# Kernel optimization log

Hardware: AMD Instinct MI355X
Metric: run time of the kernel (lower is better)

Reference implementation:

```python
import jax, jax.numpy as jnp
import numpy as np

B, L, H, HEADS, DK = 256, 20, 128, 8, 16
NT, NR = 4, 4
CHILD, PARENT = 30001, 500
N1S, N1D, E1 = 50000, 20000, 300000
N2, E2 = 20000, 200000
T = B * L
N4D, E4 = 5000, 150000
EC2P = 8000
D2 = H // 2  # gamma=0.5 split for diachronic embedding


def _ln(x):
    m = jnp.mean(x, -1, keepdims=True)
    v = jnp.var(x, -1, keepdims=True)
    return (x - m) * jax.lax.rsqrt(v + 1e-5)


def _tmod(h, w, b):
    # temporal modulation with per-node diachronic params (activ='sin')
    return jnp.concatenate([h[..., :D2], h[..., D2:] * jnp.sin(w[..., D2:] + b[..., D2:])], -1)


def _dia(e, w, b, t):
    t = t[..., None].astype(e.dtype)
    return jnp.concatenate([e[..., :D2], e[..., D2:] * jnp.sin(w[..., D2:] * t + b[..., D2:])], -1)


def _typed(x, t, W):
    # type-conditioned linear: W [NT, in, out]; small NT -> compute all, select
    y = jnp.einsum('nh,tho->tno', x, W)
    return y[t, jnp.arange(x.shape[0])]


def _seg_softmax(s, seg, n):
    m = jax.ops.segment_max(s, seg, num_segments=n)
    m = jnp.where(jnp.isfinite(m), m, 0.0)
    ex = jnp.exp(s - m[seg])
    den = jax.ops.segment_sum(ex, seg, num_segments=n)
    return ex / jnp.maximum(den[seg], 1e-9)


def _htgt(src_h, src_t, tw, tb, eh, esrc, edst, etype, dst_h, dst_t, KW, QW, VW, OW, EW, mu):
    # relational multi-head attention on a bipartite block (HTGTLayer, pre_norm)
    nd = dst_h.shape[0]
    hs = _tmod(_ln(src_h), tw, tb)
    k = _typed(hs, src_t, KW).reshape(-1, HEADS, DK)
    v = _typed(hs, src_t, VW).reshape(-1, HEADS, DK)
    q = _typed(_ln(dst_h), dst_t, QW).reshape(nd, HEADS, DK)
    ke = k[esrc] + (eh @ EW).reshape(-1, HEADS, DK)
    score = (q[edst] * ke).sum(-1) * mu[etype] / np.float32(np.sqrt(DK))  # [E, HEADS]
    a = _seg_softmax(score, edst, nd)
    agg = jax.ops.segment_sum(a[..., None] * v[esrc], edst, num_segments=nd).reshape(nd, H)
    return _typed(agg, dst_t, OW) + dst_h


def _lstm(x, Wi, Wh, b):
    h0 = jnp.zeros((x.shape[0], H), x.dtype)
    def step(carry, xt):
        h, c = carry
        g = xt @ Wi + h @ Wh + b
        i, f, gg, o = jnp.split(g, 4, -1)
        c = jax.nn.sigmoid(f) * c + jax.nn.sigmoid(i) * jnp.tanh(gg)
        h = jax.nn.sigmoid(o) * jnp.tanh(c)
        return (h, c), h
    _, hs = jax.lax.scan(step, (h0, h0), jnp.swapaxes(x, 0, 1))
    return jnp.swapaxes(hs, 0, 1)


def _forward(seq, seq_ntype, dur, stime, etime, g1_nid, g1_ntype, g1_esrc, g1_edst, g1_etype, g1_ew,
             g2_src_sel, g2_esrc, g2_edst, g2_etype, g2_ew, tok_sel, g4_esrc, g4_edst, g4_etype, g4_ew,
             pe_p, pe_c, emb, hist_emb, edge_emb, dia_w, dia_b, t2v_w, t2v_b, exp_W, exp_b,
             lstm1_Wi, lstm1_Wh, lstm1_b, lstm2_Wi, lstm2_Wh, lstm2_b,
             convK, convQ, convV, convO, convE, convMu, ipW, iaW, skip):
    # ---- sequence module ----
    e0 = emb[seq]
    st = _dia(e0, dia_w[seq], dia_b[seq], stime)
    et = _dia(e0, dia_w[seq], dia_b[seq], etime)
    t = dur[..., None].astype(jnp.float32)
    tv = jnp.concatenate([t2v_w[:1] * t + t2v_b[:1], jnp.sin(t2v_w[1:] * t + t2v_b[1:])], -1)
    x = jax.nn.relu(jnp.concatenate([st, et, tv], -1) @ exp_W + exp_b)
    h1 = _lstm(x, lstm1_Wi, lstm1_Wh, lstm1_b)
    his = jnp.swapaxes(h1, 0, 1).reshape(T, H)  # packed (time-major) token states
    tok_id = jnp.swapaxes(seq, 0, 1).reshape(T)
    tok_nt = jnp.swapaxes(seq_ntype, 0, 1).reshape(T)
    # ---- conv1 (g2g) on block 1 ----
    sh1 = emb[g1_nid]
    xg = jax.nn.relu(_htgt(sh1, g1_ntype, dia_w[g1_nid], dia_b[g1_nid], edge_emb[g1_ew],
                           g1_esrc, g1_edst, g1_etype, sh1[:N1D], g1_ntype[:N1D],
                           convK[0], convQ[0], convV[0], convO[0], convE[0], convMu[0]))
    # ---- conv2 (g2s): graph nodes -> packed sequence tokens ----
    gnid2 = g1_nid[g2_src_sel]
    dst_h2 = xg[tok_sel] + his
    x2 = jax.nn.relu(_htgt(xg[g2_src_sel], g1_ntype[g2_src_sel], dia_w[gnid2], dia_b[gnid2], edge_emb[g2_ew],
                           g2_esrc, g2_edst, g2_etype, dst_h2, tok_nt,
                           convK[1], convQ[1], convV[1], convO[1], convE[1], convMu[1]))
    seq2 = jnp.swapaxes(x2.reshape(L, B, H), 0, 1)
    h2 = _lstm(seq2, lstm2_Wi, lstm2_Wh, lstm2_b)  # final seq_embed
    # ---- individual pooling (attn) + history push ----
    ent = jnp.swapaxes(h2, 0, 1).reshape(T, H)
    a = _typed(jnp.tanh(_typed(ent, tok_nt, ipW)), tok_nt, iaW)[:, 0]
    w = _seg_softmax(a, tok_id, CHILD)
    node_embed = jax.ops.segment_sum(w[:, None] * ent, tok_id, num_segments=CHILD)
    cnt = jax.ops.segment_sum(jnp.ones((T,), jnp.float32), tok_id, num_segments=CHILD)
    hist2 = jnp.where(cnt[:, None] > 0, node_embed, hist_emb)
    # ---- graph module: conv3, conv4 with skip-gated pull ----
    alpha = jax.nn.sigmoid(skip)[g1_ntype][:, None]
    x0 = emb[g1_nid] * alpha + hist2[g1_nid] * (1.0 - alpha)
    x3 = jax.nn.relu(_htgt(x0, g1_ntype, dia_w[g1_nid], dia_b[g1_nid], edge_emb[g1_ew],
                           g1_esrc, g1_edst, g1_etype, x0[:N1D], g1_ntype[:N1D],
                           convK[2], convQ[2], convV[2], convO[2], convE[2], convMu[2]))
    nid4 = g1_nid[:N1D]
    child_embed = _htgt(x3, g1_ntype[:N1D], dia_w[nid4], dia_b[nid4], edge_emb[g4_ew],
                        g4_esrc, g4_edst, g4_etype, x3[:N4D], g1_ntype[:N4D],
                        convK[3], convQ[3], convV[3], convO[3], convE[3], convMu[3])
    # ---- parent pooling (avg over c2p map) ----
    psum = jax.ops.segment_sum(child_embed[pe_c], pe_p, num_segments=PARENT)
    pcnt = jax.ops.segment_sum(jnp.ones((EC2P,), jnp.float32), pe_p, num_segments=PARENT)
    parent_embed = psum / jnp.maximum(pcnt, 1.0)[:, None]
    return (h2, child_embed, parent_embed)


def setup_inputs() -> dict:
    key = jax.random.key(0)
    ks = iter(jax.random.split(key, 64))
    def ri(shape, hi):
        return jax.random.randint(next(ks), shape, 0, hi, dtype=jnp.int32)
    def rn(shape, s=0.02):
        return jax.random.normal(next(ks), shape, dtype=jnp.float32) * s
    return dict(
        seq=ri((B, L), CHILD), seq_ntype=ri((B, L), NT), dur=ri((B, L), 40),
        stime=ri((B, L), 60), etime=ri((B, L), 60),
        g1_nid=ri((N1S,), CHILD), g1_ntype=ri((N1S,), NT),
        g1_esrc=ri((E1,), N1S), g1_edst=ri((E1,), N1D), g1_etype=ri((E1,), NR), g1_ew=ri((E1,), 50),
        g2_src_sel=ri((N2,), N1D), g2_esrc=ri((E2,), N2), g2_edst=ri((E2,), T),
        g2_etype=ri((E2,), NR), g2_ew=ri((E2,), 50),
        tok_sel=ri((T,), N1D),
        g4_esrc=ri((E4,), N1D), g4_edst=ri((E4,), N4D), g4_etype=ri((E4,), NR), g4_ew=ri((E4,), 50),
        pe_p=ri((EC2P,), PARENT), pe_c=ri((EC2P,), N4D),
        emb=rn((CHILD, H), 0.05), hist_emb=rn((CHILD, H), 0.05), edge_emb=rn((50, 32), 0.05),
        dia_w=rn((CHILD, H), 0.05), dia_b=rn((CHILD, H), 0.05),
        t2v_w=rn((16,), 0.1), t2v_b=rn((16,), 0.1),
        exp_W=rn((2 * H + 16, H)), exp_b=jnp.zeros((H,), jnp.float32),
        lstm1_Wi=rn((H, 4 * H)), lstm1_Wh=rn((H, 4 * H)), lstm1_b=jnp.zeros((4 * H,), jnp.float32),
        lstm2_Wi=rn((H, 4 * H)), lstm2_Wh=rn((H, 4 * H)), lstm2_b=jnp.zeros((4 * H,), jnp.float32),
        convK=rn((4, NT, H, H)), convQ=rn((4, NT, H, H)), convV=rn((4, NT, H, H)), convO=rn((4, NT, H, H)),
        convE=rn((4, 32, H)), convMu=jnp.ones((4, NR, HEADS), jnp.float32),
        ipW=rn((NT, H, H)), iaW=rn((NT, H, 1)), skip=jnp.ones((NT,), jnp.float32),
    )


def reference(seq, seq_ntype, dur, stime, etime, g1_nid, g1_ntype, g1_esrc, g1_edst, g1_etype, g1_ew,
              g2_src_sel, g2_esrc, g2_edst, g2_etype, g2_ew, tok_sel, g4_esrc, g4_edst, g4_etype, g4_ew,
              pe_p, pe_c, emb, hist_emb, edge_emb, dia_w, dia_b, t2v_w, t2v_b, exp_W, exp_b,
              lstm1_Wi, lstm1_Wh, lstm1_b, lstm2_Wi, lstm2_Wh, lstm2_b,
              convK, convQ, convV, convO, convE, convMu, ipW, iaW, skip):
    return _forward(seq, seq_ntype, dur, stime, etime, g1_nid, g1_ntype, g1_esrc, g1_edst, g1_etype, g1_ew,
                    g2_src_sel, g2_esrc, g2_edst, g2_etype, g2_ew, tok_sel, g4_esrc, g4_edst, g4_etype, g4_ew,
                    pe_p, pe_c, emb, hist_emb, edge_emb, dia_w, dia_b, t2v_w, t2v_b, exp_W, exp_b,
                    lstm1_Wi, lstm1_Wh, lstm1_b, lstm2_Wi, lstm2_Wh, lstm2_b,
                    convK, convQ, convV, convO, convE, convMu, ipW, iaW, skip)
```

## Files before the change

### kernel.cpp

```cpp
#include <hip/hip_runtime.h>
#include <math.h>

#define BB 256
#define LL 20
#define HH 128
#define NH 8
#define D2C 64
#define NTY 4
#define NRL 4
#define CHILDN 30001
#define PARENTN 500
#define N1SN 50000
#define N1DN 20000
#define E1N 300000
#define N2N 20000
#define E2N 200000
#define TT (BB*LL)
#define N4DN 5000
#define E4N 150000
#define EC2PN 8000
#define TDSTRIDE 2304

typedef __attribute__((ext_vector_type(8))) short bfrag;
typedef __attribute__((ext_vector_type(4))) float ffrag;

__device__ __forceinline__ unsigned fenc(float f){ unsigned u=__float_as_uint(f); return (u&0x80000000u)? ~u : (u|0x80000000u); }
__device__ __forceinline__ float fdec(unsigned u){ return (u&0x80000000u)? __uint_as_float(u^0x80000000u) : __uint_as_float(~u); }
__device__ __forceinline__ float sigfast(float x){ return 1.f/(1.f+__expf(-x)); }
__device__ __forceinline__ float tanhfast(float x){ float e = __expf(-2.f*x); return (1.f-e)/(1.f+e); }
__device__ __forceinline__ short f2bf(float f){
  unsigned u = __float_as_uint(f);
  unsigned r = u + 0x7FFFu + ((u>>16)&1u);
  return (short)(r>>16);
}

__global__ void k_init(float* hist2, float* cnt, unsigned* amax, float* aden,
                       float* psum, float* pcnt, int* cntall,
                       int* icnt1, int* icnt2, int* icnt3,
                       const float* __restrict__ dia_w, const float* __restrict__ dia_b,
                       float* __restrict__ sdia,
                       const float* convK, const float* convV, const float* convQ,
                       const float* convO, short* Wsw,
                       const float* edge_emb, const float* convE, float* EW2all){
  int i = blockIdx.x*256 + threadIdx.x;
  if(i < CHILDN*HH) hist2[i] = 0.f;
  if(i < CHILDN){ cnt[i] = 0.f; aden[i] = 0.f; amax[i] = 0x007FFFFFu; }
  if(i < PARENTN*HH) psum[i] = 0.f;
  if(i < PARENTN) pcnt[i] = 0.f;
  if(i < 5*NTY) cntall[i] = 0;
  if(i < N1DN) icnt1[i] = 0;
  if(i < TT)   icnt2[i] = 0;
  if(i < N4DN) icnt3[i] = 0;
  if(i < CHILDN*64){
    int c = i >> 6, k = (i & 63) + 64;
    sdia[i] = __sinf(dia_w[(size_t)c*HH+k] + dia_b[(size_t)c*HH+k]);
  }
  if(i < 64*16384){
    int m = i >> 14, im = i & 16383;
    int fam = m >> 4, lt = m & 15;
    const float* src = (fam==0?convK:fam==1?convV:fam==2?convQ:convO) + (size_t)lt*HH*HH;
    int j = im & 7, lane = (im>>3)&63, kc = (im>>9)&3, nt = im>>11;
    int k = kc*32 + (lane>>4)*8 + j;
    int n = nt*16 + (lane&15);
    Wsw[(size_t)m*16384 + im] = f2bf(src[k*HH+n]);
  }
  if(i < 4*50*HH){
    int layer = i/(50*HH), rr = (i/HH)%50, o = i%HH;
    const float* EWp = convE + (size_t)layer*32*HH;
    float acc = 0.f;
    for(int j=0;j<32;j++) acc += edge_emb[rr*32+j]*EWp[j*HH+o];
    EW2all[i] = acc;
  }
}

__global__ __launch_bounds__(512) void k_featx2(const int* __restrict__ seq, const int* __restrict__ dur,
                        const int* __restrict__ stime, const int* __restrict__ etime,
                        const float* __restrict__ emb, const float* __restrict__ dia_w, const float* __restrict__ dia_b,
                        const float* __restrict__ t2v_w, const float* __restrict__ t2v_b,
                        const float* __restrict__ exp_W, const float* __restrict__ exp_b, float* __restrict__ xout){
  __shared__ float feat[32*273];
  int base = blockIdx.x*32;
  int j = threadIdx.x >> 4;
  int p = threadIdx.x & 15;
  int row = base + j;
  int node = seq[row];
  float ts = (float)stime[row], te = (float)etime[row];
  const float* ep = emb + (size_t)node*HH;
  float* fr = feat + j*273;
  int o0 = p*8;
  #pragma unroll
  for(int ii=0; ii<8; ii+=4){
    int o = o0 + ii;
    float4 e = *(const float4*)(ep + o);
    float4 st = e, et = e;
    if(o >= D2C){
      float4 w = *(const float4*)(dia_w + (size_t)node*HH + o);
      float4 b = *(const float4*)(dia_b + (size_t)node*HH + o);
      st.x = e.x*__sinf(w.x*ts+b.x); st.y = e.y*__sinf(w.y*ts+b.y);
      st.z = e.z*__sinf(w.z*ts+b.z); st.w = e.w*__sinf(w.w*ts+b.w);
      et.x = e.x*__sinf(w.x*te+b.x); et.y = e.y*__sinf(w.y*te+b.y);
      et.z = e.z*__sinf(w.z*te+b.z); et.w = e.w*__sinf(w.w*te+b.w);
    }
    fr[o] = st.x; fr[o+1] = st.y; fr[o+2] = st.z; fr[o+3] = st.w;
    fr[128+o] = et.x; fr[128+o+1] = et.y; fr[128+o+2] = et.z; fr[128+o+3] = et.w;
  }
  if(p == 0){
    float td = (float)dur[row];
    #pragma unroll
    for(int i=0;i<16;i++){
      float w = t2v_w[i], b = t2v_b[i];
      fr[256+i] = (i==0) ? (w*td + b) : __sinf(w*td + b);
    }
  }
  __syncthreads();
  int oc = (threadIdx.x & 31)*4;
  int jg = threadIdx.x >> 5;
  const float* f0 = feat + (jg*2)*273;
  const float* f1 = feat + (jg*2+1)*273;
  float4 a0 = {0,0,0,0}, a1 = {0,0,0,0};
  for(int k=0;k<272;k++){
    float4 w = *(const float4*)(exp_W + (size_t)k*HH + oc);
    float x0 = f0[k], x1 = f1[k];
    a0.x += x0*w.x; a0.y += x0*w.y; a0.z += x0*w.z; a0.w += x0*w.w;
    a1.x += x1*w.x; a1.y += x1*w.y; a1.z += x1*w.z; a1.w += x1*w.w;
  }
  float4 bv = *(const float4*)(exp_b + oc);
  a0.x = fmaxf(a0.x+bv.x, 0.f); a0.y = fmaxf(a0.y+bv.y, 0.f);
  a0.z = fmaxf(a0.z+bv.z, 0.f); a0.w = fmaxf(a0.w+bv.w, 0.f);
  a1.x = fmaxf(a1.x+bv.x, 0.f); a1.y = fmaxf(a1.y+bv.y, 0.f);
  a1.z = fmaxf(a1.z+bv.z, 0.f); a1.w = fmaxf(a1.w+bv.w, 0.f);
  *(float4*)(xout + (size_t)(base + jg*2  )*HH + oc) = a0;
  *(float4*)(xout + (size_t)(base + jg*2+1)*HH + oc) = a1;
}

__global__ void k_xwi2(const float* x, const float* Wi, const float* bias, float* gpre, int rows, int perm){
  int base = blockIdx.x*16;
  __shared__ float xs[128*17];
  int tid = threadIdx.x;
  #pragma unroll
  for(int s=0;s<8;s++){
    int elem = tid + 256*s;
    int k = elem & 127, j = elem >> 7;
    int r = base + j;
    int src = r;
    if(perm) src = (r % LL)*BB + (r / LL);
    xs[k*17 + j] = (r < rows) ? x[(size_t)src*HH + k] : 0.f;
  }
  __syncthreads();
  int o4 = (tid & 127)*4;
  int ng = tid >> 7;
  float4 a[8];
  #pragma unroll
  for(int j=0;j<8;j++) a[j]=make_float4(0,0,0,0);
  for(int k=0;k<HH;k++){
    float4 w = *(const float4*)(Wi + (size_t)k*512 + o4);
    const float* xr = xs + k*17 + ng*8;
    #pragma unroll
    for(int j=0;j<8;j++){
      float xv = xr[j];
      a[j].x += xv*w.x; a[j].y += xv*w.y; a[j].z += xv*w.z; a[j].w += xv*w.w;
    }
  }
  float4 bv = *(const float4*)(bias + o4);
  #pragma unroll
  for(int j=0;j<8;j++){
    int r = base + ng*8 + j;
    if(r < rows){
      float4 v = a[j];
      v.x += bv.x; v.y += bv.y; v.z += bv.z; v.w += bv.w;
      *(float4*)(gpre + (size_t)r*512 + o4) = v;
    }
  }
}

__global__ __launch_bounds__(512, 2) void k_lstm_fused(const float* __restrict__ gpre,
                                                       const float* __restrict__ Wh,
                                                       float* __restrict__ hout,
                                                       float* __restrict__ hout2){
  int b = blockIdx.x;
  int o = threadIdx.x;
  __shared__ float hs[HH];
  __shared__ float act[512];
  float wr[HH];
  #pragma unroll
  for(int h=0;h<HH;h++) wr[h] = Wh[(size_t)h*512 + o];
  float gv[LL];
  const float* gp = gpre + (size_t)b*LL*512 + o;
  #pragma unroll
  for(int l=0;l<LL;l++) gv[l] = gp[(size_t)l*512];
  if(o < HH) hs[o] = 0.f;
  float cc = 0.f;
  int quad = o >> 7;
  __syncthreads();
  for(int l=0;l<LL;l++){
    float a0=0.f,a1=0.f,a2=0.f,a3=0.f;
    #pragma unroll
    for(int h=0;h<HH;h+=4){
      float4 hv = *(const float4*)&hs[h];
      a0 += hv.x*wr[h];   a1 += hv.y*wr[h+1];
      a2 += hv.z*wr[h+2]; a3 += hv.w*wr[h+3];
    }
    float g = gv[l] + ((a0+a1)+(a2+a3));
    act[o] = (quad==2) ? tanhfast(g) : sigfast(g);
    __syncthreads();
    if(o < HH){
      cc = act[HH+o]*cc + act[o]*act[2*HH+o];
      float hh = act[3*HH+o]*tanhfast(cc);
      hs[o] = hh;
      size_t bi = ((size_t)b*LL + l)*HH + o;
      hout[bi] = hh;
      if(hout2) hout2[bi] = hh;
    }
    __syncthreads();
  }
}

__global__ void k_scatall(const int* __restrict__ g1_nt, const int* __restrict__ seq,
                          const int* __restrict__ seq_nt, const int* __restrict__ g2_sel,
                          const int* __restrict__ g1_nid,
                          int* __restrict__ tokid, int* __restrict__ toknt, int* __restrict__ gnid2,
                          int* __restrict__ cntall,
                          int* __restrict__ idxS1, int* __restrict__ idxS2, int* __restrict__ idxS5,
                          int* __restrict__ idxS4, int* __restrict__ idxS3,
                          const int* __restrict__ e1d, int* __restrict__ icnt1, int* __restrict__ rank1,
                          const int* __restrict__ e2d, int* __restrict__ icnt2, int* __restrict__ rank2,
                          const int* __restrict__ e3d, int* __restrict__ icnt3, int* __restrict__ rank3){
  const int B1 = (N1SN+255)/256;
  const int B2 = (TT+255)/256;
  const int B3 = (N2N+255)/256;
  const int BE1 = (E1N+255)/256;
  const int BE2 = (E2N+255)/256;
  __shared__ int h[3][NTY];
  __shared__ int bs[3][NTY];
  int bx = blockIdx.x;
  if(bx < B1){
    int i = bx*256 + threadIdx.x;
    if(threadIdx.x < 3*NTY) (&h[0][0])[threadIdx.x] = 0;
    __syncthreads();
    int t = 0, r1 = 0, r2 = 0, r3 = 0;
    bool a1 = (i < N1SN), a2 = (i < N1DN), a3 = (i < N4DN);
    if(a1){
      t = g1_nt[i];
      r1 = atomicAdd(&h[0][t], 1);
      if(a2) r2 = atomicAdd(&h[1][t], 1);
      if(a3) r3 = atomicAdd(&h[2][t], 1);
    }
    __syncthreads();
    if(threadIdx.x < NTY){
      int ty = threadIdx.x;
      if(h[0][ty] > 0) bs[0][ty] = atomicAdd(&cntall[0*NTY+ty], h[0][ty]);
      if(h[1][ty] > 0) bs[1][ty] = atomicAdd(&cntall[1*NTY+ty], h[1][ty]);
      if(h[2][ty] > 0) bs[2][ty] = atomicAdd(&cntall[4*NTY+ty], h[2][ty]);
    }
    __syncthreads();
    if(a1) idxS1[t*N1SN + bs[0][t] + r1] = i;
    if(a2) idxS2[t*N1DN + bs[1][t] + r2] = i;
    if(a3) idxS5[t*N4DN + bs[2][t] + r3] = i;
  } else if(bx < B1 + B2){
    int i = (bx - B1)*256 + threadIdx.x;
    if(threadIdx.x < NTY) h[0][threadIdx.x] = 0;
    __syncthreads();
    int nt = 0, r = 0;
    bool act = (i < TT);
    if(act){
      int b = i % BB, l = i / BB;
      tokid[i] = seq[b*LL+l];
      nt = seq_nt[b*LL+l];
      toknt[i] = nt;
      r = atomicAdd(&h[0][nt], 1);
    }
    __syncthreads();
    if(threadIdx.x < NTY && h[0][threadIdx.x] > 0)
      bs[0][threadIdx.x] = atomicAdd(&cntall[3*NTY+threadIdx.x], h[0][threadIdx.x]);
    __syncthreads();
    if(act) idxS4[nt*TT + bs[0][nt] + r] = i;
  } else if(bx < B1 + B2 + B3){
    int i = (bx - B1 - B2)*256 + threadIdx.x;
    if(threadIdx.x < NTY) h[0][threadIdx.x] = 0;
    __syncthreads();
    int nt = 0, r = 0;
    bool act = (i < N2N);
    if(act){
      int s = g2_sel[i];
      gnid2[i] = g1_nid[s];
      nt = g1_nt[s];
      r = atomicAdd(&h[0][nt], 1);
    }
    __syncthreads();
    if(threadIdx.x < NTY && h[0][threadIdx.x] > 0)
      bs[0][threadIdx.x] = atomicAdd(&cntall[2*NTY+threadIdx.x], h[0][threadIdx.x]);
    __syncthreads();
    if(act) idxS3[nt*N2N + bs[0][nt] + r] = i;
  } else if(bx < B1 + B2 + B3 + BE1){
    int e = (bx - B1 - B2 - B3)*256 + threadIdx.x;
    if(e < E1N) rank1[e] = atomicAdd(&icnt1[e1d[e]], 1);
  } else if(bx < B1 + B2 + B3 + BE1 + BE2){
    int e = (bx - B1 - B2 - B3 - BE1)*256 + threadIdx.x;
    if(e < E2N) rank2[e] = atomicAdd(&icnt2[e2d[e]], 1);
  } else {
    int e = (bx - B1 - B2 - B3 - BE1 - BE2)*256 + threadIdx.x;
    if(e < E4N) rank3[e] = atomicAdd(&icnt3[e3d[e]], 1);
  }
}

__global__ void k_dst2(const int* tok_sel, const float* xg, const float* h1, float* dst2){
  int t = blockIdx.x; int o = threadIdx.x;
  int b = t % BB, l = t / BB;
  dst2[t*HH+o] = xg[tok_sel[t]*HH+o] + h1[(b*LL+l)*HH+o];
}

__global__ void k_x0(const int* nid, const int* ntype, const float* emb, const float* hist2,
                     const float* cnt, const float* hist_emb, const float* skip, float* srcbuf){
  int i = blockIdx.x; int o = threadIdx.x;
  float a = sigfast(skip[ntype[i]]);
  int nd = nid[i];
  float hv = (cnt[nd] > 0.f) ? hist2[(size_t)nd*HH+o] : hist_emb[(size_t)nd*HH+o];
  srcbuf[i*HH+o] = emb[(size_t)nd*HH+o]*a + hv*(1.f-a);
}

__global__ void k_mktiles(const int* __restrict__ cntall, int* __restrict__ tdesc, int* __restrict__ tcnt){
  __shared__ int start[3][2][NTY];
  if(threadIdx.x == 0){
    const int srcg[3] = {0,2,1};
    const int dstg[3] = {1,3,4};
    for(int c=0;c<3;c++){
      int acc = 0;
      for(int z=0;z<2;z++){
        int g = (z==0) ? srcg[c] : dstg[c];
        int zacc = 0;
        for(int t=0;t<NTY;t++){
          start[c][z][t] = acc;
          int tiles = (cntall[g*NTY+t]+31)>>5;
          acc += tiles; zacc += tiles;
        }
        tcnt[c*2+z] = zacc;
      }
    }
  }
  __syncthreads();
  const int srcg[3] = {0,2,1};
  const int dstg[3] = {1,3,4};
  for(int c=0;c<3;c++){
    for(int z=0;z<2;z++){
      int g = (z==0) ? srcg[c] : dstg[c];
      for(int t=0;t<NTY;t++){
        int tiles = (cntall[g*NTY+t]+31)>>5;
        for(int i=threadIdx.x; i<tiles; i+=blockDim.x)
          tdesc[c*TDSTRIDE + start[c][z][t] + i] = (int)(((unsigned)z<<31) | ((unsigned)t<<28) | (unsigned)(i<<5));
      }
    }
  }
}

__global__ __launch_bounds__(256) void k_gemm_kvq(
    const int* __restrict__ tdesc, const int* __restrict__ tcnt,
    const float* __restrict__ Xs, const int* __restrict__ src_nid, const int* __restrict__ smap,
    const float* __restrict__ sdia,
    const int* __restrict__ idxs, const int* __restrict__ cnts_s, int stride_s,
    const bfrag* __restrict__ WK, const bfrag* __restrict__ WV, unsigned* __restrict__ KVp,
    const float* __restrict__ Xq, const int* __restrict__ qmap,
    const int* __restrict__ idxd, const int* __restrict__ cnts_d, int stride_d,
    const bfrag* __restrict__ WQ, float* __restrict__ Qbuf){
  __shared__ float xs[32*132];
  __shared__ float mean_s[32], inv_s[32];
  __shared__ int sid[32], nid[32], xrow[32];
  int ntk = tcnt[0], ntq = tcnt[1];
  int bid = blockIdx.x;
  if(bid >= ntk + ntq) return;
  unsigned ud = (unsigned)tdesc[bid];
  int isQ = ud >> 31;
  int t = (ud >> 28) & 7;
  int base = ud & 0x0FFFFFFF;
  int tid = threadIdx.x;
  int cnt = isQ ? cnts_d[t] : cnts_s[t];
  if(base >= cnt) return;
  int nn = min(32, cnt - base);
  const float* X = isQ ? Xq : Xs;
  const int* map = isQ ? qmap : smap;
  const int* ids = (isQ ? idxd + (size_t)t*stride_d : idxs + (size_t)t*stride_s) + base;
  if(tid < 32){
    int s_ = (tid < nn) ? ids[tid] : ids[0];
    sid[tid] = s_;
    if(!isQ) nid[tid] = src_nid[s_];
    xrow[tid] = map ? map[s_] : s_;
  }
  __syncthreads();
  #pragma unroll
  for(int s=0;s<4;s++){
    int e4 = tid + 256*s;
    int j = e4 >> 5, c4 = (e4 & 31)*4;
    *(float4*)&xs[j*132 + c4] = *(const float4*)&X[(size_t)xrow[j]*HH + c4];
  }
  __syncthreads();
  {
    int wid = tid >> 6, lane = tid & 63;
    int row = wid*8 + (lane>>3), p = lane & 7;
    const float* xr = xs + row*132 + p*16;
    float sm=0.f, sq=0.f;
    #pragma unroll
    for(int i=0;i<4;i++){
      float4 v = *(const float4*)(xr + i*4);
      sm += (v.x+v.y)+(v.z+v.w);
      sq += (v.x*v.x+v.y*v.y)+(v.z*v.z+v.w*v.w);
    }
    sm += __shfl_xor(sm, 1, 64); sq += __shfl_xor(sq, 1, 64);
    sm += __shfl_xor(sm, 2, 64); sq += __shfl_xor(sq, 2, 64);
    sm += __shfl_xor(sm, 4, 64); sq += __shfl_xor(sq, 4, 64);
    if(p == 0){
      float mean = sm*(1.f/128.f);
      float var = sq*(1.f/128.f) - mean*mean;
      mean_s[row] = mean;
      inv_s[row] = 1.f/sqrtf(fmaxf(var,0.f)+1e-5f);
    }
  }
  __syncthreads();
  #pragma unroll
  for(int s=0;s<4;s++){
    int e4 = tid + 256*s;
    int j = e4 >> 5, c4 = (e4 & 31)*4;
    float* px = &xs[j*132 + c4];
    float4 v = *(float4*)px;
    float mj = mean_s[j], ij = inv_s[j];
    v.x = (v.x-mj)*ij; v.y = (v.y-mj)*ij; v.z = (v.z-mj)*ij; v.w = (v.w-mj)*ij;
    if(!isQ && c4 >= D2C){
      float4 sd = *(const float4*)(sdia + (size_t)nid[j]*64 + (c4 - D2C));
      v.x *= sd.x; v.y *= sd.y; v.z *= sd.z; v.w *= sd.w;
    }
    *(float4*)px = v;
  }
  __syncthreads();
  int lane = tid & 63, w = tid >> 6;
  int mt = w & 1, ng0 = (w>>1)*4;
  int arow = mt*16 + (lane & 15);
  int koff = (lane >> 4)*8;
  int tb = t*2048;
  if(!isQ){
    ffrag aK[4], aV[4];
    #pragma unroll
    for(int i=0;i<4;i++){ aK[i] = (ffrag){0.f,0.f,0.f,0.f}; aV[i] = (ffrag){0.f,0.f,0.f,0.f}; }
    #pragma unroll
    for(int kc=0;kc<4;kc++){
      const float* ap = xs + arow*132 + kc*32 + koff;
      bfrag a;
      #pragma unroll
      for(int j=0;j<8;j++) a[j] = f2bf(ap[j]);
      #pragma unroll
      for(int nt=0;nt<4;nt++){
        int fi = tb + ((ng0+nt)*4 + kc)*64 + lane;
        bfrag bk = WK[fi];
        bfrag bv = WV[fi];
        aK[nt] = __builtin_amdgcn_mfma_f32_16x16x32_bf16(a, bk, aK[nt], 0, 0, 0);
        aV[nt] = __builtin_amdgcn_mfma_f32_16x16x32_bf16(a, bv, aV[nt], 0, 0, 0);
      }
    }
    int col0 = lane & 15;
    int rb = mt*16 + (lane>>4)*4;
    #pragma unroll
    for(int nt=0;nt<4;nt++){
      int col = (ng0+nt)*16 + col0;
      #pragma unroll
      for(int i=0;i<4;i++){
        int n = rb + i;
        if(n < nn){
          unsigned pk = (unsigned short)f2bf(aK[nt][i]);
          unsigned pv = (unsigned short)f2bf(aV[nt][i]);
          KVp[(size_t)sid[n]*HH + col] = (pv<<16) | pk;
        }
      }
    }
  } else {
    ffrag acc[4];
    #pragma unroll
    for(int i=0;i<4;i++) acc[i] = (ffrag){0.f,0.f,0.f,0.f};
    #pragma unroll
    for(int kc=0;kc<4;kc++){
      const float* ap = xs + arow*132 + kc*32 + koff;
      bfrag a;
      #pragma unroll
      for(int j=0;j<8;j++) a[j] = f2bf(ap[j]);
      #pragma unroll
      for(int nt=0;nt<4;nt++){
        bfrag b = WQ[tb + ((ng0+nt)*4 + kc)*64 + lane];
        acc[nt] = __builtin_amdgcn_mfma_f32_16x16x32_bf16(a, b, acc[nt], 0, 0, 0);
      }
    }
    int col0 = lane & 15;
    int rb = mt*16 + (lane>>4)*4;
    #pragma unroll
    for(int nt=0;nt<4;nt++){
      int col = (ng0+nt)*16 + col0;
      #pragma unroll
      for(int i=0;i<4;i++){
        int n = rb + i;
        if(n < nn) Qbuf[(size_t)sid[n]*HH + col] = acc[nt][i];
      }
    }
  }
}

__global__ __launch_bounds__(256) void k_gemm_t5(
    const int* __restrict__ tdesc, const int* __restrict__ tcnt,
    const float* X, const int* idxb, const int* cnts, int stride,
    const bfrag* W, const float* resid, const int* rmap, float* Y, float* Y2,
    int relu){
  __shared__ float xs[32*132];
  __shared__ int sid[32], rrow[32];
  int ntk = tcnt[0], ntq = tcnt[1];
  if(blockIdx.x >= ntq) return;
  unsigned ud = (unsigned)tdesc[ntk + blockIdx.x];
  int t = (ud >> 28) & 7;
  int base = ud & 0x0FFFFFFF;
  int cnt = cnts[t];
  if(base >= cnt) return;
  int nn = min(32, cnt - base);
  const int* ids = idxb + (size_t)t*stride + base;
  int tid = threadIdx.x;
  if(tid < 32){
    int s_ = (tid < nn) ? ids[tid] : ids[0];
    sid[tid] = s_;
    rrow[tid] = rmap ? rmap[s_] : s_;
  }
  __syncthreads();
  #pragma unroll
  for(int s=0;s<4;s++){
    int e4 = tid + 256*s;
    int j = e4 >> 5, c4 = (e4 & 31)*4;
    *(float4*)&xs[j*132 + c4] = *(const float4*)&X[(size_t)sid[j]*HH + c4];
  }
  __syncthreads();
  int lane = tid & 63, w = tid >> 6;
  int mt = w & 1, ng0 = (w>>1)*4;
  int arow = mt*16 + (lane & 15);
  int koff = (lane >> 4)*8;
  int tb = t*2048;
  ffrag acc[4];
  #pragma unroll
  for(int i=0;i<4;i++) acc[i] = (ffrag){0.f,0.f,0.f,0.f};
  #pragma unroll
  for(int kc=0;kc<4;kc++){
    const float* ap = xs + arow*132 + kc*32 + koff;
    bfrag a;
    #pragma unroll
    for(int j=0;j<8;j++) a[j] = f2bf(ap[j]);
    #pragma unroll
    for(int nt=0;nt<4;nt++){
      bfrag b = W[tb + ((ng0+nt)*4 + kc)*64 + lane];
      acc[nt] = __builtin_amdgcn_mfma_f32_16x16x32_bf16(a, b, acc[nt], 0, 0, 0);
    }
  }
  int col0 = lane & 15;
  int rb = mt*16 + (lane>>4)*4;
  #pragma unroll
  for(int nt=0;nt<4;nt++){
    int col = (ng0+nt)*16 + col0;
    #pragma unroll
    for(int i=0;i<4;i++){
      int n = rb + i;
      if(n < nn){
        size_t r = (size_t)sid[n]*HH + col;
        float v = acc[nt][i];
        if(resid){
          v += resid[(size_t)rrow[n]*HH + col];
          if(relu) v = fmaxf(v, 0.f);
        }
        Y[r] = v;
        if(Y2) Y2[r] = v;
      }
    }
  }
}

__global__ void k_scan3(const int* c1, int n1, int* r1,
                        const int* c2, int n2, int* r2,
                        const int* c3, int n3, int* r3){
  __shared__ int tsum[1024];
  const int* cnt; int n; int* row_ptr;
  if(blockIdx.x == 0){ cnt=c1; n=n1; row_ptr=r1; }
  else if(blockIdx.x == 1){ cnt=c2; n=n2; row_ptr=r2; }
  else { cnt=c3; n=n3; row_ptr=r3; }
  int tid = threadIdx.x;
  int per = (n + 1023) / 1024;
  int start = tid*per; int end = min(start+per, n);
  int s = 0;
  for(int i=start;i<end;i++) s += cnt[i];
  tsum[tid] = s; __syncthreads();
  for(int off=1;off<1024;off<<=1){
    int v = (tid>=off) ? tsum[tid-off] : 0;
    __syncthreads();
    tsum[tid] += v;
    __syncthreads();
  }
  int run = (tid==0) ? 0 : tsum[tid-1];
  for(int i=start;i<end;i++){ row_ptr[i]=run; run += cnt[i]; }
  if(end == n) row_ptr[n] = run;
}
__global__ void k_fillperm3(const int* d1, const int* s1, const int* w1, const int* t1,
                            const int* rp1, const int* rk1, int2* m1,
                            const int* d2, const int* s2, const int* w2, const int* t2,
                            const int* rp2, const int* rk2, int2* m2,
                            const int* d3, const int* s3, const int* w3, const int* t3,
                            const int* rp3, const int* rk3, int2* m3){
  const int B1 = (E1N+255)/256, B2 = (E2N+255)/256;
  int bx = blockIdx.x;
  if(bx < B1){
    int e = bx*256 + threadIdx.x;
    if(e < E1N){ int pos = rp1[d1[e]] + rk1[e]; m1[pos] = make_int2(s1[e], w1[e] | (t1[e]<<16)); }
  } else if(bx < B1+B2){
    int e = (bx-B1)*256 + threadIdx.x;
    if(e < E2N){ int pos = rp2[d2[e]] + rk2[e]; m2[pos] = make_int2(s2[e], w2[e] | (t2[e]<<16)); }
  } else {
    int e = (bx-B1-B2)*256 + threadIdx.x;
    if(e < E4N){ int pos = rp3[d3[e]] + rk3[e]; m3[pos] = make_int2(s3[e], w3[e] | (t3[e]<<16)); }
  }
}

__global__ void k_attn_fused8(const int* __restrict__ row_ptr, const int2* __restrict__ meta,
                              const unsigned* __restrict__ KVp, const float* __restrict__ Qbuf,
                              const float* __restrict__ EW2, const float* __restrict__ mu,
                              float* __restrict__ Abuf){
  int d = blockIdx.x; int o = threadIdx.x;
  int r0 = row_ptr[d], r1 = row_ptr[d+1];
  __shared__ float q[HH];
  q[o] = Qbuf[(size_t)d*HH+o]*0.25f;
  __syncthreads();
  int h = o >> 4;
  float qo = q[o];
  float dn0=0.f, dn1=0.f, dn2=0.f, dn3=0.f;
  float ac0=0.f, ac1=0.f, ac2=0.f, ac3=0.f;
  int r = r0;
  for(; r+7 < r1; r += 8){
    int2 m[8]; unsigned u[8]; float e[8]; float p[8];
    #pragma unroll
    for(int j=0;j<8;j++) m[j] = meta[r+j];
    #pragma unroll
    for(int j=0;j<8;j++) u[j] = KVp[(size_t)m[j].x*HH + o];
    #pragma unroll
    for(int j=0;j<8;j++) e[j] = EW2[(m[j].y & 0xffff)*HH + o];
    #pragma unroll
    for(int j=0;j<8;j++) p[j] = qo*(__uint_as_float(u[j]<<16) + e[j]);
    #pragma unroll
    for(int j=0;j<8;j++) p[j] += __shfl_xor(p[j], 1, 64);
    #pragma unroll
    for(int j=0;j<8;j++) p[j] += __shfl_xor(p[j], 2, 64);
    #pragma unroll
    for(int j=0;j<8;j++) p[j] += __shfl_xor(p[j], 4, 64);
    #pragma unroll
    for(int j=0;j<8;j++) p[j] += __shfl_xor(p[j], 8, 64);
    float ex[8];
    #pragma unroll
    for(int j=0;j<8;j++) ex[j] = __expf(p[j]*mu[(m[j].y>>16)*NH+h]);
    dn0 += ex[0]+ex[4]; dn1 += ex[1]+ex[5]; dn2 += ex[2]+ex[6]; dn3 += ex[3]+ex[7];
    ac0 += ex[0]*__uint_as_float(u[0]&0xffff0000u) + ex[4]*__uint_as_float(u[4]&0xffff0000u);
    ac1 += ex[1]*__uint_as_float(u[1]&0xffff0000u) + ex[5]*__uint_as_float(u[5]&0xffff0000u);
    ac2 += ex[2]*__uint_as_float(u[2]&0xffff0000u) + ex[6]*__uint_as_float(u[6]&0xffff0000u);
    ac3 += ex[3]*__uint_as_float(u[3]&0xffff0000u) + ex[7]*__uint_as_float(u[7]&0xffff0000u);
  }
  for(; r+3 < r1; r += 4){
    int2 m[4]; unsigned u[4]; float e[4]; float p[4];
    #pragma unroll
    for(int j=0;j<4;j++) m[j] = meta[r+j];
    #pragma unroll
    for(int j=0;j<4;j++) u[j] = KVp[(size_t)m[j].x*HH + o];
    #pragma unroll
    for(int j=0;j<4;j++) e[j] = EW2[(m[j].y & 0xffff)*HH + o];
    #pragma unroll
    for(int j=0;j<4;j++) p[j] = qo*(__uint_as_float(u[j]<<16) + e[j]);
    #pragma unroll
    for(int j=0;j<4;j++) p[j] += __shfl_xor(p[j], 1, 64);
    #pragma unroll
    for(int j=0;j<4;j++) p[j] += __shfl_xor(p[j], 2, 64);
    #pragma unroll
    for(int j=0;j<4;j++) p[j] += __shfl_xor(p[j], 4, 64);
    #pragma unroll
    for(int j=0;j<4;j++) p[j] += __shfl_xor(p[j], 8, 64);
    float ex[4];
    #pragma unroll
    for(int j=0;j<4;j++) ex[j] = __expf(p[j]*mu[(m[j].y>>16)*NH+h]);
    dn0 += ex[0]; dn1 += ex[1]; dn2 += ex[2]; dn3 += ex[3];
    ac0 += ex[0]*__uint_as_float(u[0]&0xffff0000u);
    ac1 += ex[1]*__uint_as_float(u[1]&0xffff0000u);
    ac2 += ex[2]*__uint_as_float(u[2]&0xffff0000u);
    ac3 += ex[3]*__uint_as_float(u[3]&0xffff0000u);
  }
  for(; r < r1; r++){
    int2 m = meta[r];
    unsigned u = KVp[(size_t)m.x*HH + o];
    float p = qo*(__uint_as_float(u<<16) + EW2[(m.y & 0xffff)*HH + o]);
    p += __shfl_xor(p, 1, 64);
    p += __shfl_xor(p, 2, 64);
    p += __shfl_xor(p, 4, 64);
    p += __shfl_xor(p, 8, 64);
    float ex = __expf(p*mu[(m.y>>16)*NH+h]);
    dn0 += ex; ac0 += ex*__uint_as_float(u&0xffff0000u);
  }
  float dd = (dn0+dn1)+(dn2+dn3), acc = (ac0+ac1)+(ac2+ac3);
  Abuf[(size_t)d*HH + o] = acc / fmaxf(dd, 1e-9f);
}

__global__ void k_tokatt(const float* h2f, const int* toknt, const float* ipW, const float* iaW,
                         float* abuf, unsigned* amax, const int* tokid){
  int t = blockIdx.x; int o = threadIdx.x;
  __shared__ float es[HH];
  __shared__ float red[HH];
  int b = t % BB, l = t / BB;
  es[o] = h2f[(b*LL+l)*HH+o];
  __syncthreads();
  int nt = toknt[t];
  const float* w = ipW + (size_t)nt*HH*HH;
  float acc = 0.f;
  for(int j=0;j<HH;j++) acc += es[j]*w[j*HH+o];
  float u = tanhfast(acc);
  red[o] = u * iaW[nt*HH+o];
  __syncthreads();
  for(int s=64;s>0;s>>=1){ if(o<s) red[o]+=red[o+s]; __syncthreads(); }
  if(o==0){
    float a = red[0];
    abuf[t] = a;
    atomicMax(&amax[tokid[t]], fenc(a));
  }
}

__global__ void k_tokexp(const int* tokid, float* abuf, const unsigned* amax, float* aden, float* cnt){
  int t = blockIdx.x*blockDim.x + threadIdx.x;
  if(t >= TT) return;
  int c = tokid[t];
  float ex = __expf(abuf[t]-fdec(amax[c]));
  abuf[t] = ex;
  atomicAdd(&aden[c], ex);
  atomicAdd(&cnt[c], 1.f);
}

__global__ void k_tokagg(const int* tokid, const float* abuf, const float* aden,
                         const float* h2f, float* hist2){
  int t = blockIdx.x; int o = threadIdx.x;
  int c = tokid[t];
  float w = abuf[t]/fmaxf(aden[c],1e-9f);
  int b = t % BB, l = t / BB;
  atomicAdd(&hist2[c*HH+o], w*h2f[(b*LL+l)*HH+o]);
}

__global__ void k_peagg(const int* pe_p, const int* pe_c, const float* cef, float* psum, float* pcnt){
  int i = blockIdx.x; int o = threadIdx.x;
  int p = pe_p[i], c = pe_c[i];
  atomicAdd(&psum[p*HH+o], cef[c*HH+o]);
  if(o==0) atomicAdd(&pcnt[p], 1.f);
}

__global__ void k_parent(const float* psum, const float* pcnt, float* out){
  int i = blockIdx.x; int o = threadIdx.x;
  out[i*HH+o] = psum[i*HH+o]/fmaxf(pcnt[i],1.f);
}

extern "C" void kernel_launch(void* const* d_in, const int* in_sizes, int n_in,
                              void* d_out, int out_size, void* d_ws, size_t ws_size,
                              hipStream_t stream){
  const int* seq     = (const int*)d_in[0];
  const int* seq_nt  = (const int*)d_in[1];
  const int* dur     = (const int*)d_in[2];
  const int* stime   = (const int*)d_in[3];
  const int* etime   = (const int*)d_in[4];
  const int* g1_nid  = (const int*)d_in[5];
  const int* g1_nt   = (const int*)d_in[6];
  const int* g1_esrc = (const int*)d_in[7];
  const int* g1_edst = (const int*)d_in[8];
  const int* g1_ety  = (const int*)d_in[9];
  const int* g1_ew   = (const int*)d_in[10];
  const int* g2_sel  = (const int*)d_in[11];
  const int* g2_esrc = (const int*)d_in[12];
  const int* g2_edst = (const int*)d_in[13];
  const int* g2_ety  = (const int*)d_in[14];
  const int* g2_ew   = (const int*)d_in[15];
  const int* tok_sel = (const int*)d_in[16];
  const int* g4_esrc = (const int*)d_in[17];
  const int* g4_edst = (const int*)d_in[18];
  const int* g4_ety  = (const int*)d_in[19];
  const int* g4_ew   = (const int*)d_in[20];
  const int* pe_p    = (const int*)d_in[21];
  const int* pe_c    = (const int*)d_in[22];
  const float* emb     = (const float*)d_in[23];
  const float* hist_emb= (const float*)d_in[24];
  const float* edge_emb= (const float*)d_in[25];
  const float* dia_w   = (const float*)d_in[26];
  const float* dia_b   = (const float*)d_in[27];
  const float* t2v_w   = (const float*)d_in[28];
  const float* t2v_b   = (const float*)d_in[29];
  const float* exp_W   = (const float*)d_in[30];
  const float* exp_b   = (const float*)d_in[31];
  const float* l1Wi    = (const float*)d_in[32];
  const float* l1Wh    = (const float*)d_in[33];
  const float* l1b     = (const float*)d_in[34];
  const float* l2Wi    = (const float*)d_in[35];
  const float* l2Wh    = (const float*)d_in[36];
  const float* l2b     = (const float*)d_in[37];
  const float* convK   = (const float*)d_in[38];
  const float* convQ   = (const float*)d_in[39];
  const float* convV   = (const float*)d_in[40];
  const float* convO   = (const float*)d_in[41];
  const float* convE   = (const float*)d_in[42];
  const float* convMu  = (const float*)d_in[43];
  const float* ipW     = (const float*)d_in[44];
  const float* iaW     = (const float*)d_in[45];
  const float* skip    = (const float*)d_in[46];
  float* outp = (float*)d_out;

  char* wsp = (char*)d_ws;
  size_t off = 0;
  auto A = [&](size_t nbytes)->char*{ char* p = wsp+off; off += (nbytes+255)&~(size_t)255; return p; };
  float*    srcbuf = (float*)   A((size_t)N1SN*HH*4);
  unsigned* KVp    = (unsigned*)A((size_t)N1SN*HH*4);
  float*    Qbuf   = (float*)   A((size_t)N1DN*HH*4);
  float*    Abuf   = (float*)   A((size_t)N1DN*HH*4);
  float*    xbuf   = (float*)   A((size_t)TT*HH*4);
  float*    gpre   = (float*)   A((size_t)TT*512*4);
  float*    h1     = (float*)   A((size_t)TT*HH*4);
  float*    dst2   = (float*)   A((size_t)TT*HH*4);
  float*    xg     = (float*)   A((size_t)N1DN*HH*4);
  float*    x2     = (float*)   A((size_t)TT*HH*4);
  float*    h2f    = (float*)   A((size_t)TT*HH*4);
  float*    hist2  = (float*)   A((size_t)CHILDN*HH*4);
  float*    cnt    = (float*)   A((size_t)CHILDN*4);
  float*    abuf   = (float*)   A((size_t)TT*4);
  unsigned* amax   = (unsigned*)A((size_t)CHILDN*4);
  float*    aden   = (float*)   A((size_t)CHILDN*4);
  float*    x3     = (float*)   A((size_t)N1DN*HH*4);
  float*    cef    = (float*)   A((size_t)N4DN*HH*4);
  float*    psum   = (float*)   A((size_t)PARENTN*HH*4);
  float*    pcnt   = (float*)   A((size_t)PARENTN*4);
  float*    sdia   = (float*)   A((size_t)CHILDN*64*4);
  int*      tokid  = (int*)     A((size_t)TT*4);
  int*      toknt  = (int*)     A((size_t)TT*4);
  int*      gnid2  = (int*)     A((size_t)N2N*4);
  int*      idxS1  = (int*)     A((size_t)NTY*N1SN*4);
  int*      idxS2  = (int*)     A((size_t)NTY*N1DN*4);
  int*      idxS3  = (int*)     A((size_t)NTY*N2N*4);
  int*      idxS4  = (int*)     A((size_t)NTY*TT*4);
  int*      idxS5  = (int*)     A((size_t)NTY*N4DN*4);
  int*      cntall = (int*)     A((size_t)5*NTY*4);
  int*      tdesc  = (int*)     A((size_t)3*TDSTRIDE*4);
  int*      tcnt   = (int*)     A((size_t)8*4);
  float*    EW2all = (float*)   A((size_t)4*50*HH*4);
  short*    Wsw    = (short*)   A((size_t)64*16384*2);
  int*      g1row  = (int*)     A((size_t)(N1DN+1)*4);
  int2*     g1meta = (int2*)    A((size_t)E1N*8);
  int*      g1rank = (int*)     A((size_t)E1N*4);
  int*      g2row  = (int*)     A((size_t)(TT+1)*4);
  int2*     g2meta = (int2*)    A((size_t)E2N*8);
  int*      g2rank = (int*)     A((size_t)E2N*4);
  int*      g4row  = (int*)     A((size_t)(N4DN+1)*4);
  int2*     g4meta = (int2*)    A((size_t)E4N*8);
  int*      g4rank = (int*)     A((size_t)E4N*4);
  int*      icnt1  = (int*)     A((size_t)(N1DN+1)*4);
  int*      icnt2  = (int*)     A((size_t)(TT+1)*4);
  int*      icnt3  = (int*)     A((size_t)(N4DN+1)*4);
  if(off > ws_size) return;

  auto run_conv = [&](int cfg, int gkvq, int gq,
                      const float* src_X, const int* src_nid, const int* srcmap,
                      const int* idx_src, int* cnt_src, int stride_src,
                      const float* q_X, const int* q_map,
                      const float* resid_X, const int* r_map, int ndst,
                      const int* idx_dst, int* cnt_dst, int stride_dst,
                      const int* rowp, const int2* meta,
                      int layer, float* outbuf, float* out2, int relu){
    const bfrag* WB = (const bfrag*)Wsw;
    const bfrag* WK = WB + (size_t)( 0 + layer*4)*2048;
    const bfrag* WV = WB + (size_t)(16 + layer*4)*2048;
    const bfrag* WQ = WB + (size_t)(32 + layer*4)*2048;
    const bfrag* WO = WB + (size_t)(48 + layer*4)*2048;
    const float* MU  = convMu + (size_t)layer*NRL*NH;
    const float* EW2 = EW2all + (size_t)layer*50*HH;
    const int* td = tdesc + (size_t)cfg*TDSTRIDE;
    const int* tc = tcnt + cfg*2;
    k_gemm_kvq<<<gkvq, 256, 0, stream>>>(td, tc, src_X, src_nid, srcmap, sdia,
                                         idx_src, cnt_src, stride_src, WK, WV, KVp,
                                         q_X, q_map, idx_dst, cnt_dst, stride_dst, WQ, Qbuf);
    k_attn_fused8<<<ndst, HH, 0, stream>>>(rowp, meta, KVp, Qbuf, EW2, MU, Abuf);
    k_gemm_t5<<<gq, 256, 0, stream>>>(td, tc, Abuf, idx_dst, cnt_dst, stride_dst, WO,
                                      resid_X, r_map, outbuf, out2, relu);
  };

  k_init<<<(CHILDN*HH+255)/256, 256, 0, stream>>>(hist2, cnt, amax, aden, psum, pcnt, cntall,
                                                  icnt1, icnt2, icnt3,
                                                  dia_w, dia_b, sdia,
                                                  convK, convV, convQ, convO, Wsw,
                                                  edge_emb, convE, EW2all);
  {
    const int B1 = (N1SN+255)/256, B2 = (TT+255)/256, B3 = (N2N+255)/256;
    const int BE1 = (E1N+255)/256, BE2 = (E2N+255)/256, BE3 = (E4N+255)/256;
    k_scatall<<<B1+B2+B3+BE1+BE2+BE3, 256, 0, stream>>>(g1_nt, seq, seq_nt, g2_sel, g1_nid,
                                            tokid, toknt, gnid2, cntall,
                                            idxS1, idxS2, idxS5, idxS4, idxS3,
                                            g1_edst, icnt1, g1rank,
                                            g2_edst, icnt2, g2rank,
                                            g4_edst, icnt3, g4rank);
  }
  k_mktiles<<<1, 256, 0, stream>>>(cntall, tdesc, tcnt);
  k_scan3<<<3, 1024, 0, stream>>>(icnt1, N1DN, g1row,
                                  icnt2, TT,   g2row,
                                  icnt3, N4DN, g4row);
  {
    const int BE1 = (E1N+255)/256, BE2 = (E2N+255)/256, BE3 = (E4N+255)/256;
    k_fillperm3<<<BE1+BE2+BE3, 256, 0, stream>>>(g1_edst, g1_esrc, g1_ew, g1_ety, g1row, g1rank, g1meta,
                                                 g2_edst, g2_esrc, g2_ew, g2_ety, g2row, g2rank, g2meta,
                                                 g4_edst, g4_esrc, g4_ew, g4_ety, g4row, g4rank, g4meta);
  }

  k_featx2<<<TT/32, 512, 0, stream>>>(seq, dur, stime, etime, emb, dia_w, dia_b, t2v_w, t2v_b, exp_W, exp_b, xbuf);
  k_xwi2<<<(TT+15)/16, 256, 0, stream>>>(xbuf, l1Wi, l1b, gpre, TT, 0);
  k_lstm_fused<<<BB, 512, 0, stream>>>(gpre, l1Wh, h1, (float*)nullptr);

  const int GKVQ_A = (N1SN+N1DN)/32 + 8;
  const int GKVQ_B = (N2N+TT)/32 + 8;
  const int GKVQ_C = (N1DN+N4DN)/32 + 8;
  const int GQ_A   = (N1DN+31)/32 + 4;
  const int GQ_B   = (TT+31)/32 + 4;
  const int GQ_C   = (N4DN+31)/32 + 4;

  run_conv(0, GKVQ_A, GQ_A,
           emb, g1_nid, g1_nid, idxS1, cntall+0*NTY, N1SN,
           emb, g1_nid,
           emb, g1_nid, N1DN, idxS2, cntall+1*NTY, N1DN,
           g1row, g1meta, 0, xg, (float*)nullptr, 1);

  k_dst2<<<TT, HH, 0, stream>>>(tok_sel, xg, h1, dst2);
  run_conv(1, GKVQ_B, GQ_B,
           xg, gnid2, g2_sel, idxS3, cntall+2*NTY, N2N,
           dst2, (const int*)nullptr,
           dst2, (const int*)nullptr, TT, idxS4, cntall+3*NTY, TT,
           g2row, g2meta, 1, x2, (float*)nullptr, 1);

  k_xwi2<<<(TT+15)/16, 256, 0, stream>>>(x2, l2Wi, l2b, gpre, TT, 1);
  k_lstm_fused<<<BB, 512, 0, stream>>>(gpre, l2Wh, h2f, outp);

  k_tokatt<<<TT, HH, 0, stream>>>(h2f, toknt, ipW, iaW, abuf, amax, tokid);
  k_tokexp<<<(TT+255)/256, 256, 0, stream>>>(tokid, abuf, amax, aden, cnt);
  k_tokagg<<<TT, HH, 0, stream>>>(tokid, abuf, aden, h2f, hist2);

  k_x0<<<N1SN, HH, 0, stream>>>(g1_nid, g1_nt, emb, hist2, cnt, hist_emb, skip, srcbuf);
  run_conv(0, GKVQ_A, GQ_A,
           srcbuf, g1_nid, (const int*)nullptr, idxS1, cntall+0*NTY, N1SN,
           srcbuf, (const int*)nullptr,
           srcbuf, (const int*)nullptr, N1DN, idxS2, cntall+1*NTY, N1DN,
           g1row, g1meta, 2, x3, (float*)nullptr, 1);

  run_conv(2, GKVQ_C, GQ_C,
           x3, g1_nid, (const int*)nullptr, idxS2, cntall+1*NTY, N1DN,
           x3, (const int*)nullptr,
           x3, (const int*)nullptr, N4DN, idxS5, cntall+4*NTY, N4DN,
           g4row, g4meta, 3, cef, outp + (size_t)TT*HH, 0);

  k_peagg<<<EC2PN, HH, 0, stream>>>(pe_p, pe_c, cef, psum, pcnt);
  k_parent<<<PARENTN, HH, 0, stream>>>(psum, pcnt, outp + (size_t)TT*HH + (size_t)N4DN*HH);
}
```

Before: 696.3 us.

## Compute token attention projection with bf16 MFMA over type-grouped token tiles

```diff
diff --git a/kernel.cpp b/kernel.cpp
--- a/kernel.cpp
+++ b/kernel.cpp
@@ -41,6 +41,7 @@
                        float* __restrict__ sdia,
                        const float* convK, const float* convV, const float* convQ,
                        const float* convO, short* Wsw,
+                       const float* ipW, short* WswI,
                        const float* edge_emb, const float* convE, float* EW2all){
   int i = blockIdx.x*256 + threadIdx.x;
   if(i < CHILDN*HH) hist2[i] = 0.f;
@@ -63,6 +64,14 @@
     int k = kc*32 + (lane>>4)*8 + j;
     int n = nt*16 + (lane&15);
     Wsw[(size_t)m*16384 + im] = f2bf(src[k*HH+n]);
+  }
+  if(i < 4*16384){
+    int m = i >> 14, im = i & 16383;
+    const float* src = ipW + (size_t)m*HH*HH;
+    int j = im & 7, lane = (im>>3)&63, kc = (im>>9)&3, nt = im>>11;
+    int k = kc*32 + (lane>>4)*8 + j;
+    int n = nt*16 + (lane&15);
+    WswI[(size_t)m*16384 + im] = f2bf(src[k*HH+n]);
   }
   if(i < 4*50*HH){
     int layer = i/(50*HH), rr = (i/HH)%50, o = i%HH;
@@ -570,6 +579,88 @@
   }
 }
 
+__global__ __launch_bounds__(256) void k_tokatt2(
+    const int* __restrict__ tdesc, const int* __restrict__ tcnt,
+    const float* __restrict__ h2f, const int* __restrict__ idxd, const int* __restrict__ cnts_d,
+    const bfrag* __restrict__ WI, const float* __restrict__ iaW,
+    const int* __restrict__ tokid, float* __restrict__ abuf, unsigned* __restrict__ amax){
+  __shared__ float xs[32*132];
+  __shared__ float red[32];
+  __shared__ int sid[32];
+  int ntk = tcnt[0], ntq = tcnt[1];
+  if(blockIdx.x >= ntq) return;
+  unsigned ud = (unsigned)tdesc[ntk + blockIdx.x];
+  int t = (ud >> 28) & 7;
+  int base = ud & 0x0FFFFFFF;
+  int cnt = cnts_d[t];
+  if(base >= cnt) return;
+  int nn = min(32, cnt - base);
+  const int* ids = idxd + (size_t)t*TT + base;
+  int tid = threadIdx.x;
+  if(tid < 32){
+    sid[tid] = (tid < nn) ? ids[tid] : ids[0];
+    red[tid] = 0.f;
+  }
+  __syncthreads();
+  #pragma unroll
+  for(int s=0;s<4;s++){
+    int e4 = tid + 256*s;
+    int j = e4 >> 5, c4 = (e4 & 31)*4;
+    int tok = sid[j];
+    int b = tok % BB, l = tok / BB;
+    *(float4*)&xs[j*132 + c4] = *(const float4*)&h2f[((size_t)(b*LL+l))*HH + c4];
+  }
+  __syncthreads();
+  int lane = tid & 63, w = tid >> 6;
+  int mt = w & 1, ng0 = (w>>1)*4;
+  int arow = mt*16 + (lane & 15);
+  int koff = (lane >> 4)*8;
+  int tb = t*2048;
+  ffrag acc[4];
+  #pragma unroll
+  for(int i=0;i<4;i++) acc[i] = (ffrag){0.f,0.f,0.f,0.f};
+  #pragma unroll
+  for(int kc=0;kc<4;kc++){
+    const float* ap = xs + arow*132 + kc*32 + koff;
+    bfrag a;
+    #pragma unroll
+    for(int j=0;j<8;j++) a[j] = f2bf(ap[j]);
+    #pragma unroll
+    for(int nt=0;nt<4;nt++){
+      bfrag b = WI[tb + ((ng0+nt)*4 + kc)*64 + lane];
+      acc[nt] = __builtin_amdgcn_mfma_f32_16x16x32_bf16(a, b, acc[nt], 0, 0, 0);
+    }
+  }
+  int col0 = lane & 15;
+  int rb = mt*16 + (lane>>4)*4;
+  float rsum[4] = {0.f, 0.f, 0.f, 0.f};
+  #pragma unroll
+  for(int nt=0;nt<4;nt++){
+    int col = (ng0+nt)*16 + col0;
+    float wia = iaW[t*HH + col];
+    #pragma unroll
+    for(int i=0;i<4;i++) rsum[i] += tanhfast(acc[nt][i]) * wia;
+  }
+  #pragma unroll
+  for(int i=0;i<4;i++){
+    rsum[i] += __shfl_xor(rsum[i], 1, 64);
+    rsum[i] += __shfl_xor(rsum[i], 2, 64);
+    rsum[i] += __shfl_xor(rsum[i], 4, 64);
+    rsum[i] += __shfl_xor(rsum[i], 8, 64);
+  }
+  if(col0 == 0){
+    #pragma unroll
+    for(int i=0;i<4;i++) atomicAdd(&red[rb+i], rsum[i]);
+  }
+  __syncthreads();
+  if(tid < nn){
+    int tok = sid[tid];
+    float a = red[tid];
+    abuf[tok] = a;
+    atomicMax(&amax[tokid[tok]], fenc(a));
+  }
+}
+
 __global__ void k_scan3(const int* c1, int n1, int* r1,
                         const int* c2, int n2, int* r2,
                         const int* c3, int n3, int* r3){
@@ -695,29 +786,6 @@
   }
   float dd = (dn0+dn1)+(dn2+dn3), acc = (ac0+ac1)+(ac2+ac3);
   Abuf[(size_t)d*HH + o] = acc / fmaxf(dd, 1e-9f);
-}
-
-__global__ void k_tokatt(const float* h2f, const int* toknt, const float* ipW, const float* iaW,
-                         float* abuf, unsigned* amax, const int* tokid){
-  int t = blockIdx.x; int o = threadIdx.x;
-  __shared__ float es[HH];
-  __shared__ float red[HH];
-  int b = t % BB, l = t / BB;
-  es[o] = h2f[(b*LL+l)*HH+o];
-  __syncthreads();
-  int nt = toknt[t];
-  const float* w = ipW + (size_t)nt*HH*HH;
-  float acc = 0.f;
-  for(int j=0;j<HH;j++) acc += es[j]*w[j*HH+o];
-  float u = tanhfast(acc);
-  red[o] = u * iaW[nt*HH+o];
-  __syncthreads();
-  for(int s=64;s>0;s>>=1){ if(o<s) red[o]+=red[o+s]; __syncthreads(); }
-  if(o==0){
-    float a = red[0];
-    abuf[t] = a;
-    atomicMax(&amax[tokid[t]], fenc(a));
-  }
 }
 
 __global__ void k_tokexp(const int* tokid, float* abuf, const unsigned* amax, float* aden, float* cnt){
@@ -840,6 +908,7 @@
   int*      tcnt   = (int*)     A((size_t)8*4);
   float*    EW2all = (float*)   A((size_t)4*50*HH*4);
   short*    Wsw    = (short*)   A((size_t)64*16384*2);
+  short*    WswI   = (short*)   A((size_t)4*16384*2);
   int*      g1row  = (int*)     A((size_t)(N1DN+1)*4);
   int2*     g1meta = (int2*)    A((size_t)E1N*8);
   int*      g1rank = (int*)     A((size_t)E1N*4);
@@ -883,6 +952,7 @@
                                                   icnt1, icnt2, icnt3,
                                                   dia_w, dia_b, sdia,
                                                   convK, convV, convQ, convO, Wsw,
+                                                  ipW, WswI,
                                                   edge_emb, convE, EW2all);
   {
     const int B1 = (N1SN+255)/256, B2 = (TT+255)/256, B3 = (N2N+255)/256;
@@ -932,7 +1002,9 @@
   k_xwi2<<<(TT+15)/16, 256, 0, stream>>>(x2, l2Wi, l2b, gpre, TT, 1);
   k_lstm_fused<<<BB, 512, 0, stream>>>(gpre, l2Wh, h2f, outp);
 
-  k_tokatt<<<TT, HH, 0, stream>>>(h2f, toknt, ipW, iaW, abuf, amax, tokid);
+  k_tokatt2<<<GQ_B, 256, 0, stream>>>(tdesc + (size_t)1*TDSTRIDE, tcnt + 2,
+                                      h2f, idxS4, cntall+3*NTY,
+                                      (const bfrag*)WswI, iaW, tokid, abuf, amax);
   k_tokexp<<<(TT+255)/256, 256, 0, stream>>>(tokid, abuf, amax, aden, cnt);
   k_tokagg<<<TT, HH, 0, stream>>>(tokid, abuf, aden, h2f, hist2);
 
```

Result: faster. 678.9 us (-2.5%).
